# Optimization experiments

Measured on AMD Instinct MI355X. Metric: run time of the kernel, lower is better.

The kernel has to match this reference:

```python
import jax, jax.numpy as jnp
import numpy as np

B, T, D, U = 64, 512, 512, 1024
LN_EPS = 1e-3  # keras LayerNormalization default


def setup_inputs() -> dict:
    key = jax.random.key(0)
    ks = jax.random.split(key, 6)
    s = 0.02
    return {
        "x": jax.random.normal(ks[0], (B, T, D), jnp.float32),
        "W1": jax.random.normal(ks[1], (D, 4 * U), jnp.float32) * s,
        "R1": jax.random.normal(ks[2], (U, 4 * U), jnp.float32) * s,
        "b1": jnp.zeros((4 * U,), jnp.float32),
        "gamma1": jnp.ones((U,), jnp.float32),
        "beta1": jnp.zeros((U,), jnp.float32),
        "W2": jax.random.normal(ks[3], (U, 4 * U), jnp.float32) * s,
        "R2": jax.random.normal(ks[4], (U, 4 * U), jnp.float32) * s,
        "b2": jnp.zeros((4 * U,), jnp.float32),
        "gamma2": jnp.ones((U,), jnp.float32),
        "beta2": jnp.zeros((U,), jnp.float32),
    }


def lstm_linear(x_btd, W, R, b, return_sequences):
    """Keras LSTM with activation=None: i,f,o sigmoid gates, identity candidate/output."""
    units = R.shape[0]
    # Precompute input projection for all timesteps: [B,T,4U]
    zx = jnp.einsum('btd,dk->btk', x_btd, W) + b

    def step(carry, zx_t):
        h, c = carry
        z = zx_t + h @ R  # [B,4U]
        zi, zf, zg, zo = jnp.split(z, 4, axis=-1)
        i = jax.nn.sigmoid(zi)
        f = jax.nn.sigmoid(zf)
        o = jax.nn.sigmoid(zo)
        c = f * c + i * zg          # activation=None -> linear candidate
        h = o * c                   # activation=None -> linear output
        return (h, c), h

    bsz = x_btd.shape[0]
    init = (jnp.zeros((bsz, units), x_btd.dtype), jnp.zeros((bsz, units), x_btd.dtype))
    (h_last, _), hs = jax.lax.scan(step, init, jnp.swapaxes(zx, 0, 1))  # hs: [T,B,U]
    return jnp.swapaxes(hs, 0, 1) if return_sequences else h_last


def layernorm(x, gamma, beta, eps=LN_EPS):
    mu = jnp.mean(x, axis=-1, keepdims=True)
    var = jnp.mean(jnp.square(x - mu), axis=-1, keepdims=True)
    return (x - mu) * jax.lax.rsqrt(var + eps) * gamma + beta


def reference(x, W1, R1, b1, gamma1, beta1, W2, R2, b2, gamma2, beta2):
    # Layer 1: LSTM (return_sequences=True) -> LayerNorm -> tanh
    h = lstm_linear(x, W1, R1, b1, return_sequences=True)   # [B,T,U]
    h = jnp.tanh(layernorm(h, gamma1, beta1))
    # Layer 2: LSTM (return_sequences=False) -> LayerNorm -> tanh
    h = lstm_linear(h, W2, R2, b2, return_sequences=False)  # [B,U]
    h = jnp.tanh(layernorm(h, gamma2, beta2))
    return h
```

## Files before the change

kernel.cpp:

```cpp
#include <hip/hip_runtime.h>
#include <stdint.h>

#define B_ 64
#define T_ 512
#define D_ 512
#define U_ 1024
#define TC 32
#define NCH 16

typedef unsigned short u16;
typedef u16 ushort8  __attribute__((ext_vector_type(8)));
typedef __bf16 bf16x8 __attribute__((ext_vector_type(8)));
typedef float f32x4  __attribute__((ext_vector_type(4)));

static __device__ __forceinline__ u16 f2bf(float f) {
  unsigned u = __builtin_bit_cast(unsigned, f);
  u += 0x7FFFu + ((u >> 16) & 1u);
  return (u16)(u >> 16);
}
static __device__ __forceinline__ float bf2f(u16 h) {
  unsigned u = ((unsigned)h) << 16;
  return __builtin_bit_cast(float, u);
}


__global__ __launch_bounds__(256) void pack_wt(const float* __restrict__ src,
                                               u16* __restrict__ dst, int K) {
  __shared__ float tile[32][33];
  int n0 = blockIdx.x * 32, k0 = blockIdx.y * 32;
  int tx = threadIdx.x, ty = threadIdx.y;
#pragma unroll
  for (int r = 0; r < 4; ++r) {
    int k = k0 + ty + r * 8;
    tile[ty + r * 8][tx] = src[(long)k * 4096 + n0 + tx];
  }
  __syncthreads();
#pragma unroll
  for (int r = 0; r < 4; ++r) {
    int n = n0 + ty + r * 8;
    int np = ((n & 1023) << 2) | (n >> 10);
    dst[(long)np * K + k0 + tx] = f2bf(tile[tx][ty + r * 8]);
  }
}

__global__ __launch_bounds__(256) void pack_bias(const float* __restrict__ b1,
                                                 const float* __restrict__ b2,
                                                 float* __restrict__ bp) {
  int n = blockIdx.x * 256 + threadIdx.x;
  int np = ((n & 1023) << 2) | (n >> 10);
  bp[np] = b1[n];
  bp[4096 + np] = b2[n];
}


template <bool AF32>
__global__ __launch_bounds__(512) void zx_gemm(const void* __restrict__ Av, long sB, long sT,
                                               int K, const u16* __restrict__ Bp,
                                               const float* __restrict__ biasp,
                                               float* __restrict__ zxo) {
  __shared__ __align__(16) u16 Als[128][72];
  __shared__ __align__(16) u16 Bls[128][72];
  const int tid = threadIdx.x;
  const int mt = blockIdx.x, nt = blockIdx.y;
  const int l = tid & 63, w = tid >> 6;
  const int wm = w >> 2, wn = w & 3;
  const int sr = tid >> 2, skq = (tid & 3) * 16;

  const int gr = mt * 128 + sr;
  const int b = gr >> 5, tt = gr & 31;
  const long abase = (long)b * sB + (long)tt * sT;
  const float* Af = (const float*)Av;
  const u16* Ah = (const u16*)Av;

  const int nc = K >> 6;
  float4 raf[4];
  ushort8 rah[2];
  ushort8 rb[2];

  auto gload = [&](int ch) {
    long k0 = (long)ch << 6;
    if constexpr (AF32) {
#pragma unroll
      for (int i = 0; i < 4; ++i)
        raf[i] = *reinterpret_cast<const float4*>(Af + abase + k0 + skq + i * 4);
    } else {
#pragma unroll
      for (int i = 0; i < 2; ++i)
        rah[i] = *reinterpret_cast<const ushort8*>(Ah + abase + k0 + skq + i * 8);
    }
#pragma unroll
    for (int i = 0; i < 2; ++i)
      rb[i] = *reinterpret_cast<const ushort8*>(Bp + (long)(nt * 128 + sr) * K + k0 + skq + i * 8);
  };

  f32x4 acc[4][2];
#pragma unroll
  for (int fm = 0; fm < 4; ++fm)
#pragma unroll
    for (int fn = 0; fn < 2; ++fn) acc[fm][fn] = (f32x4){0.f, 0.f, 0.f, 0.f};

  gload(0);
  for (int ch = 0; ch < nc; ++ch) {
    __syncthreads();
    if constexpr (AF32) {
      const float* pr = (const float*)raf;
      ushort8 lo, hi;
#pragma unroll
      for (int j = 0; j < 8; ++j) { lo[j] = f2bf(pr[j]); hi[j] = f2bf(pr[8 + j]); }
      *reinterpret_cast<ushort8*>(&Als[sr][skq]) = lo;
      *reinterpret_cast<ushort8*>(&Als[sr][skq + 8]) = hi;
    } else {
      *reinterpret_cast<ushort8*>(&Als[sr][skq]) = rah[0];
      *reinterpret_cast<ushort8*>(&Als[sr][skq + 8]) = rah[1];
    }
    *reinterpret_cast<ushort8*>(&Bls[sr][skq]) = rb[0];
    *reinterpret_cast<ushort8*>(&Bls[sr][skq + 8]) = rb[1];
    __syncthreads();
    if (ch + 1 < nc) gload(ch + 1);
#pragma unroll
    for (int ks = 0; ks < 2; ++ks) {
#pragma unroll
      for (int fm = 0; fm < 4; ++fm) {
        bf16x8 a = __builtin_bit_cast(bf16x8,
            *reinterpret_cast<const ushort8*>(&Als[wm * 64 + fm * 16 + (l & 15)][ks * 32 + (l >> 4) * 8]));
#pragma unroll
        for (int fn = 0; fn < 2; ++fn) {
          bf16x8 bb = __builtin_bit_cast(bf16x8,
              *reinterpret_cast<const ushort8*>(&Bls[wn * 32 + fn * 16 + (l & 15)][ks * 32 + (l >> 4) * 8]));
          acc[fm][fn] = __builtin_amdgcn_mfma_f32_16x16x32_bf16(a, bb, acc[fm][fn], 0, 0, 0);
        }
      }
    }
  }

#pragma unroll
  for (int fm = 0; fm < 4; ++fm)
#pragma unroll
    for (int fn = 0; fn < 2; ++fn) {
      int col = nt * 128 + wn * 32 + fn * 16 + (l & 15);
      float bv = biasp[col];
#pragma unroll
      for (int j = 0; j < 4; ++j) {
        int row = mt * 128 + wm * 64 + fm * 16 + (l >> 4) * 4 + j;
        zxo[(long)row * 4096 + col] = acc[fm][fn][j] + bv;
      }
    }
}


__global__ __launch_bounds__(512) void step2(
    const float* __restrict__ zx1, const u16* __restrict__ R1p, float* __restrict__ c1v,
    const u16* __restrict__ h1r, u16* __restrict__ h1w, u16* __restrict__ h1s,
    const float* __restrict__ zx2, const u16* __restrict__ R2p, float* __restrict__ c2v,
    const u16* __restrict__ h2r, u16* __restrict__ h2w,
    int tt, int act1, int act2) {
  const int layer = blockIdx.x >> 7;
  if (layer ? (!act2) : (!act1)) return;

  __shared__ __align__(16) u16 Als[64][136];
  __shared__ __align__(16) u16 Bls[32][136];
  __shared__ float Zls[64][36];

  const float* zx = layer ? zx2 : zx1;
  const u16* Rp   = layer ? R2p : R1p;
  float* cv       = layer ? c2v : c1v;
  const u16* hr   = layer ? h2r : h1r;
  u16* hw         = layer ? h2w : h1w;

  const int cb = blockIdx.x & 127;
  const int n0 = cb * 32;
  const int tid = threadIdx.x;
  const int l = tid & 63, w = tid >> 6;
  const int wm = w >> 1, wn = w & 1;

  const int arow = tid >> 3, ak = (tid & 7) * 16;
  const int brow = tid >> 4, bk = (tid & 15) * 8;

  ushort8 ra0, ra1, rbv;
  auto gload = [&](int ch) {
    const int k0 = ch << 7;
    ra0 = *reinterpret_cast<const ushort8*>(hr + arow * U_ + k0 + ak);
    ra1 = *reinterpret_cast<const ushort8*>(hr + arow * U_ + k0 + ak + 8);
    rbv = *reinterpret_cast<const ushort8*>(Rp + (long)(n0 + brow) * U_ + k0 + bk);
  };

  f32x4 acc = {0.f, 0.f, 0.f, 0.f};
  gload(0);
  for (int ch = 0; ch < 8; ++ch) {
    __syncthreads();
    *reinterpret_cast<ushort8*>(&Als[arow][ak]) = ra0;
    *reinterpret_cast<ushort8*>(&Als[arow][ak + 8]) = ra1;
    *reinterpret_cast<ushort8*>(&Bls[brow][bk]) = rbv;
    __syncthreads();
    if (ch < 7) gload(ch + 1);
#pragma unroll
    for (int ks = 0; ks < 4; ++ks) {
      bf16x8 a = __builtin_bit_cast(bf16x8,
          *reinterpret_cast<const ushort8*>(&Als[wm * 16 + (l & 15)][ks * 32 + (l >> 4) * 8]));
      bf16x8 bb = __builtin_bit_cast(bf16x8,
          *reinterpret_cast<const ushort8*>(&Bls[wn * 16 + (l & 15)][ks * 32 + (l >> 4) * 8]));
      acc = __builtin_amdgcn_mfma_f32_16x16x32_bf16(a, bb, acc, 0, 0, 0);
    }
  }

  {
    int r0 = (l >> 4) * 4, col = wn * 16 + (l & 15);
#pragma unroll
    for (int j = 0; j < 4; ++j) Zls[wm * 16 + r0 + j][col] = acc[j];
  }
  __syncthreads();

  {
    int b = tid >> 3, uu = tid & 7;
    int u = cb * 8 + uu;
    float z0 = Zls[b][uu * 4], z1 = Zls[b][uu * 4 + 1];
    float z2 = Zls[b][uu * 4 + 2], z3 = Zls[b][uu * 4 + 3];
    f32x4 zv = *reinterpret_cast<const f32x4*>(zx + ((long)b * TC + tt) * 4096 + n0 + uu * 4);
    float zi = z0 + zv[0], zf = z1 + zv[1], zg = z2 + zv[2], zo = z3 + zv[3];
    float ig = 1.f / (1.f + expf(-zi));
    float fg = 1.f / (1.f + expf(-zf));
    float og = 1.f / (1.f + expf(-zo));
    long ci = (long)b * U_ + u;
    float cn = fg * cv[ci] + ig * zg;
    cv[ci] = cn;
    u16 hv = f2bf(og * cn);
    hw[ci] = hv;
    if (layer == 0) h1s[(long)b * ((long)T_ * U_) + u] = hv;
  }
}


__global__ __launch_bounds__(256) void ln_chunk(const u16* __restrict__ h1seq, int t0,
                                                const float* __restrict__ gamma,
                                                const float* __restrict__ beta,
                                                u16* __restrict__ dst) {
  __shared__ float sbuf[8];
  int row = blockIdx.x;
  int b = row >> 5, tt = row & 31;
  const u16* src = h1seq + ((long)b * T_ + t0 + tt) * U_;
  u16* drow = dst + (long)row * U_;
  float x[4];
#pragma unroll
  for (int j = 0; j < 4; ++j) x[j] = bf2f(src[threadIdx.x + 256 * j]);
  float s = x[0] + x[1] + x[2] + x[3];
  for (int o = 32; o > 0; o >>= 1) s += __shfl_down(s, o, 64);
  if ((threadIdx.x & 63) == 0) sbuf[threadIdx.x >> 6] = s;
  __syncthreads();
  float mu = (sbuf[0] + sbuf[1] + sbuf[2] + sbuf[3]) * (1.f / 1024.f);
  float d[4], s2 = 0.f;
#pragma unroll
  for (int j = 0; j < 4; ++j) { d[j] = x[j] - mu; s2 += d[j] * d[j]; }
  for (int o = 32; o > 0; o >>= 1) s2 += __shfl_down(s2, o, 64);
  if ((threadIdx.x & 63) == 0) sbuf[4 + (threadIdx.x >> 6)] = s2;
  __syncthreads();
  float inv = rsqrtf((sbuf[4] + sbuf[5] + sbuf[6] + sbuf[7]) * (1.f / 1024.f) + 1e-3f);
#pragma unroll
  for (int j = 0; j < 4; ++j) {
    int u = threadIdx.x + 256 * j;
    drow[u] = f2bf(tanhf(d[j] * inv * gamma[u] + beta[u]));
  }
}

__global__ __launch_bounds__(256) void ln_tanh_final(const u16* __restrict__ h2,
                                                     const float* __restrict__ gamma,
                                                     const float* __restrict__ beta,
                                                     float* __restrict__ out) {
  __shared__ float sbuf[8];
  const u16* row = h2 + (long)blockIdx.x * U_;
  float x[4];
#pragma unroll
  for (int j = 0; j < 4; ++j) x[j] = bf2f(row[threadIdx.x + 256 * j]);
  float s = x[0] + x[1] + x[2] + x[3];
  for (int o = 32; o > 0; o >>= 1) s += __shfl_down(s, o, 64);
  if ((threadIdx.x & 63) == 0) sbuf[threadIdx.x >> 6] = s;
  __syncthreads();
  float mu = (sbuf[0] + sbuf[1] + sbuf[2] + sbuf[3]) * (1.f / 1024.f);
  float d[4], s2 = 0.f;
#pragma unroll
  for (int j = 0; j < 4; ++j) { d[j] = x[j] - mu; s2 += d[j] * d[j]; }
  for (int o = 32; o > 0; o >>= 1) s2 += __shfl_down(s2, o, 64);
  if ((threadIdx.x & 63) == 0) sbuf[4 + (threadIdx.x >> 6)] = s2;
  __syncthreads();
  float inv = rsqrtf((sbuf[4] + sbuf[5] + sbuf[6] + sbuf[7]) * (1.f / 1024.f) + 1e-3f);
#pragma unroll
  for (int j = 0; j < 4; ++j) {
    int u = threadIdx.x + 256 * j;
    out[(long)blockIdx.x * U_ + u] = tanhf(d[j] * inv * gamma[u] + beta[u]);
  }
}


extern "C" void kernel_launch(void* const* d_in, const int* in_sizes, int n_in,
                              void* d_out, int out_size, void* d_ws, size_t ws_size,
                              hipStream_t stream) {
  const float* x      = (const float*)d_in[0];
  const float* W1     = (const float*)d_in[1];
  const float* R1     = (const float*)d_in[2];
  const float* b1     = (const float*)d_in[3];
  const float* gamma1 = (const float*)d_in[4];
  const float* beta1  = (const float*)d_in[5];
  const float* W2     = (const float*)d_in[6];
  const float* R2     = (const float*)d_in[7];
  const float* b2     = (const float*)d_in[8];
  const float* gamma2 = (const float*)d_in[9];
  const float* beta2  = (const float*)d_in[10];
  float* out = (float*)d_out;

  char* base = (char*)d_ws;
  size_t off = 0;
  auto alloc = [&](size_t bytes) -> void* {
    void* p = base + off;
    off += (bytes + 255) & ~(size_t)255;
    return p;
  };
  u16*   Wp1   = (u16*)alloc((size_t)4096 * D_ * 2);
  u16*   Rp1   = (u16*)alloc((size_t)4096 * U_ * 2);
  u16*   Wp2   = (u16*)alloc((size_t)4096 * U_ * 2);
  u16*   Rp2   = (u16*)alloc((size_t)4096 * U_ * 2);
  float* biasp = (float*)alloc((size_t)2 * 4096 * 4);
  float* zxA   = (float*)alloc((size_t)B_ * TC * 4096 * 4);
  float* zxB   = (float*)alloc((size_t)B_ * TC * 4096 * 4);
  u16*   h1seq = (u16*)alloc((size_t)B_ * T_ * U_ * 2);
  u16*   h1ln  = (u16*)alloc((size_t)B_ * TC * U_ * 2);
  float* c1    = (float*)alloc((size_t)B_ * U_ * 4);
  float* c2    = (float*)alloc((size_t)B_ * U_ * 4);
  u16*   h1a   = (u16*)alloc((size_t)B_ * U_ * 2);
  u16*   h1b   = (u16*)alloc((size_t)B_ * U_ * 2);
  u16*   h2a   = (u16*)alloc((size_t)B_ * U_ * 2);
  u16*   h2b   = (u16*)alloc((size_t)B_ * U_ * 2);

  pack_wt<<<dim3(128, 16), dim3(32, 8), 0, stream>>>(W1, Wp1, D_);
  pack_wt<<<dim3(128, 32), dim3(32, 8), 0, stream>>>(R1, Rp1, U_);
  pack_wt<<<dim3(128, 32), dim3(32, 8), 0, stream>>>(W2, Wp2, U_);
  pack_wt<<<dim3(128, 32), dim3(32, 8), 0, stream>>>(R2, Rp2, U_);
  pack_bias<<<16, 256, 0, stream>>>(b1, b2, biasp);
  hipMemsetAsync(c1, 0, (size_t)B_ * U_ * 4, stream);
  hipMemsetAsync(c2, 0, (size_t)B_ * U_ * 4, stream);
  hipMemsetAsync(h1a, 0, (size_t)B_ * U_ * 2, stream);
  hipMemsetAsync(h2a, 0, (size_t)B_ * U_ * 2, stream);

  for (int p = 0; p <= NCH; ++p) {
    int act1 = (p < NCH), act2 = (p >= 1);
    if (act1)
      zx_gemm<true><<<dim3(16, 32), 512, 0, stream>>>(
          (const void*)(x + (long)p * TC * D_), (long)T_ * D_, (long)D_, D_, Wp1, biasp, zxA);
    if (act2) {
      ln_chunk<<<B_ * TC, 256, 0, stream>>>(h1seq, (p - 1) * TC, gamma1, beta1, h1ln);
      zx_gemm<false><<<dim3(16, 32), 512, 0, stream>>>(
          (const void*)h1ln, (long)TC * U_, (long)U_, U_, Wp2, biasp + 4096, zxB);
    }
    for (int tt = 0; tt < TC; ++tt) {
      u16* h1r = (tt & 1) ? h1b : h1a;
      u16* h1w = (tt & 1) ? h1a : h1b;
      u16* h2r = (tt & 1) ? h2b : h2a;
      u16* h2w = (tt & 1) ? h2a : h2b;
      step2<<<256, 512, 0, stream>>>(zxA, Rp1, c1, h1r, h1w,
                                     h1seq + (long)(p * TC + tt) * U_,
                                     zxB, Rp2, c2, h2r, h2w, tt, act1, act2);
    }
  }
  ln_tanh_final<<<B_, 256, 0, stream>>>(h2a, gamma2, beta2, out);
}
```

Measured before the change: 5.370 ms.

## Replace per-timestep launches with persistent cooperative chunk kernel using flag sync

Each 32-step chunk now runs as one cooperative kernel of 256 blocks instead of 32 separate step launches. Blocks synchronize between timesteps through per-step atomic counters that are spin-polled. Each block keeps its cell state in a register and now covers 16 batch rows by 128 gate columns, with double-buffered recurrent-weight tiles. This is meant to remove launch overhead and the round-trip of c through global memory, at the cost of spin-wait latency and a reliance on all blocks being co-resident.

New measurement: 6.276 ms. 16.9% more time.

```diff
diff --git a/kernel.cpp b/kernel.cpp
--- a/kernel.cpp
+++ b/kernel.cpp
@@ -9,6 +9,7 @@
 #define NCH 16
 
 typedef unsigned short u16;
+typedef unsigned long long u64;
 typedef u16 ushort8  __attribute__((ext_vector_type(8)));
 typedef __bf16 bf16x8 __attribute__((ext_vector_type(8)));
 typedef float f32x4  __attribute__((ext_vector_type(4)));
@@ -148,85 +149,129 @@
 }
 
 
-__global__ __launch_bounds__(512) void step2(
+__global__ __launch_bounds__(512) void lstm_chunk(
     const float* __restrict__ zx1, const u16* __restrict__ R1p, float* __restrict__ c1v,
-    const u16* __restrict__ h1r, u16* __restrict__ h1w, u16* __restrict__ h1s,
+    u16* __restrict__ h1_0, u16* __restrict__ h1_1, u16* __restrict__ h1s,
     const float* __restrict__ zx2, const u16* __restrict__ R2p, float* __restrict__ c2v,
-    const u16* __restrict__ h2r, u16* __restrict__ h2w,
-    int tt, int act1, int act2) {
+    u16* __restrict__ h2_0, u16* __restrict__ h2_1,
+    unsigned* __restrict__ flag1, unsigned* __restrict__ flag2,
+    int g01, int g02, int act1, int act2) {
   const int layer = blockIdx.x >> 7;
   if (layer ? (!act2) : (!act1)) return;
 
-  __shared__ __align__(16) u16 Als[64][136];
-  __shared__ __align__(16) u16 Bls[32][136];
-  __shared__ float Zls[64][36];
+  __shared__ __align__(16) u16 Als[16][1032];
+  __shared__ __align__(16) u16 Bls[2][128][136];
+  __shared__ float Zls[16][132];
 
   const float* zx = layer ? zx2 : zx1;
   const u16* Rp   = layer ? R2p : R1p;
   float* cv       = layer ? c2v : c1v;
-  const u16* hr   = layer ? h2r : h1r;
-  u16* hw         = layer ? h2w : h1w;
-
-  const int cb = blockIdx.x & 127;
-  const int n0 = cb * 32;
+  u16* hb0        = layer ? h2_0 : h1_0;
+  u16* hb1        = layer ? h2_1 : h1_1;
+  unsigned* flag  = layer ? flag2 : flag1;
+  const int g0    = layer ? g02 : g01;
+
+  const int lb = blockIdx.x & 127;
+  const int q = lb >> 5;
+  const int cg = lb & 31;
+  const int n0 = cg * 128;
+  const int u0 = cg * 32;
+
   const int tid = threadIdx.x;
   const int l = tid & 63, w = tid >> 6;
-  const int wm = w >> 1, wn = w & 1;
-
-  const int arow = tid >> 3, ak = (tid & 7) * 16;
-  const int brow = tid >> 4, bk = (tid & 15) * 8;
-
-  ushort8 ra0, ra1, rbv;
-  auto gload = [&](int ch) {
-    const int k0 = ch << 7;
-    ra0 = *reinterpret_cast<const ushort8*>(hr + arow * U_ + k0 + ak);
-    ra1 = *reinterpret_cast<const ushort8*>(hr + arow * U_ + k0 + ak + 8);
-    rbv = *reinterpret_cast<const ushort8*>(Rp + (long)(n0 + brow) * U_ + k0 + bk);
+
+  const int tArow = tid >> 5, tAoff = (tid & 31) * 32;
+  const int tBrow = tid >> 2, tBoff = (tid & 3) * 32;
+  const int tgb = tid >> 5, tgun = tid & 31;
+  const int bq = q * 16 + tgb;
+  const int ug = u0 + tgun;
+
+  float creg = cv[(long)bq * U_ + ug];
+
+  ushort8 rbv[4];
+  auto gloadB = [&](int ch) {
+#pragma unroll
+    for (int i = 0; i < 4; ++i)
+      rbv[i] = *reinterpret_cast<const ushort8*>(Rp + (long)(n0 + tBrow) * U_ + ch * 128 + tBoff + i * 8);
   };
 
-  f32x4 acc = {0.f, 0.f, 0.f, 0.f};
-  gload(0);
-  for (int ch = 0; ch < 8; ++ch) {
+  for (int tt = 0; tt < TC; ++tt) {
+    const int g = g0 + tt;
+
+    if (g > 0) {
+      if (tid == 0) {
+        while (__hip_atomic_load(&flag[g - 1], __ATOMIC_RELAXED, __HIP_MEMORY_SCOPE_AGENT) < 128u)
+          __builtin_amdgcn_s_sleep(2);
+      }
+      __syncthreads();
+    }
+
+    const u16* hr = (g & 1) ? hb0 : hb1;
+    u16* hw       = (g & 1) ? hb1 : hb0;
+    {
+      u64* src = (u64*)(hr + (long)(q * 16 + tArow) * U_ + tAoff);
+#pragma unroll
+      for (int i = 0; i < 8; ++i) {
+        u64 v = __hip_atomic_load(src + i, __ATOMIC_RELAXED, __HIP_MEMORY_SCOPE_AGENT);
+        *reinterpret_cast<u64*>(&Als[tArow][tAoff + i * 4]) = v;
+      }
+    }
+
+    f32x4 acc = {0.f, 0.f, 0.f, 0.f};
+    gloadB(0);
+#pragma unroll
+    for (int i = 0; i < 4; ++i)
+      *reinterpret_cast<ushort8*>(&Bls[0][tBrow][tBoff + i * 8]) = rbv[i];
+    for (int ch = 0; ch < 8; ++ch) {
+      if (ch < 7) gloadB(ch + 1);
+      __syncthreads();
+      if (ch < 7) {
+#pragma unroll
+        for (int i = 0; i < 4; ++i)
+          *reinterpret_cast<ushort8*>(&Bls[(ch + 1) & 1][tBrow][tBoff + i * 8]) = rbv[i];
+      }
+#pragma unroll
+      for (int ks = 0; ks < 4; ++ks) {
+        bf16x8 a = __builtin_bit_cast(bf16x8,
+            *reinterpret_cast<const ushort8*>(&Als[l & 15][ch * 128 + ks * 32 + (l >> 4) * 8]));
+        bf16x8 bb = __builtin_bit_cast(bf16x8,
+            *reinterpret_cast<const ushort8*>(&Bls[ch & 1][w * 16 + (l & 15)][ks * 32 + (l >> 4) * 8]));
+        acc = __builtin_amdgcn_mfma_f32_16x16x32_bf16(a, bb, acc, 0, 0, 0);
+      }
+    }
+
+    {
+      int r0 = (l >> 4) * 4, col = w * 16 + (l & 15);
+#pragma unroll
+      for (int j = 0; j < 4; ++j) Zls[r0 + j][col] = acc[j];
+    }
     __syncthreads();
-    *reinterpret_cast<ushort8*>(&Als[arow][ak]) = ra0;
-    *reinterpret_cast<ushort8*>(&Als[arow][ak + 8]) = ra1;
-    *reinterpret_cast<ushort8*>(&Bls[brow][bk]) = rbv;
+
+    {
+      f32x4 zr = *reinterpret_cast<const f32x4*>(&Zls[tgb][tgun * 4]);
+      f32x4 zv = *reinterpret_cast<const f32x4*>(zx + ((long)bq * TC + tt) * 4096 + n0 + tgun * 4);
+      float zi = zr[0] + zv[0], zf = zr[1] + zv[1], zg = zr[2] + zv[2], zo = zr[3] + zv[3];
+      float ig = 1.f / (1.f + expf(-zi));
+      float fg = 1.f / (1.f + expf(-zf));
+      float og = 1.f / (1.f + expf(-zo));
+      creg = fg * creg + ig * zg;
+      u16 hv = f2bf(og * creg);
+      unsigned hvn = __shfl_down((unsigned)hv, 1, 64);
+      if ((tgun & 1) == 0) {
+        unsigned pv = (unsigned)hv | (hvn << 16);
+        __hip_atomic_store((unsigned*)(hw + (long)bq * U_ + ug), pv,
+                           __ATOMIC_RELAXED, __HIP_MEMORY_SCOPE_AGENT);
+      }
+      if (layer == 0) h1s[((long)bq * T_ + g) * U_ + ug] = hv;
+    }
+
+    asm volatile("s_waitcnt vmcnt(0)" ::: "memory");
     __syncthreads();
-    if (ch < 7) gload(ch + 1);
-#pragma unroll
-    for (int ks = 0; ks < 4; ++ks) {
-      bf16x8 a = __builtin_bit_cast(bf16x8,
-          *reinterpret_cast<const ushort8*>(&Als[wm * 16 + (l & 15)][ks * 32 + (l >> 4) * 8]));
-      bf16x8 bb = __builtin_bit_cast(bf16x8,
-          *reinterpret_cast<const ushort8*>(&Bls[wn * 16 + (l & 15)][ks * 32 + (l >> 4) * 8]));
-      acc = __builtin_amdgcn_mfma_f32_16x16x32_bf16(a, bb, acc, 0, 0, 0);
-    }
-  }
-
-  {
-    int r0 = (l >> 4) * 4, col = wn * 16 + (l & 15);
-#pragma unroll
-    for (int j = 0; j < 4; ++j) Zls[wm * 16 + r0 + j][col] = acc[j];
-  }
-  __syncthreads();
-
-  {
-    int b = tid >> 3, uu = tid & 7;
-    int u = cb * 8 + uu;
-    float z0 = Zls[b][uu * 4], z1 = Zls[b][uu * 4 + 1];
-    float z2 = Zls[b][uu * 4 + 2], z3 = Zls[b][uu * 4 + 3];
-    f32x4 zv = *reinterpret_cast<const f32x4*>(zx + ((long)b * TC + tt) * 4096 + n0 + uu * 4);
-    float zi = z0 + zv[0], zf = z1 + zv[1], zg = z2 + zv[2], zo = z3 + zv[3];
-    float ig = 1.f / (1.f + expf(-zi));
-    float fg = 1.f / (1.f + expf(-zf));
-    float og = 1.f / (1.f + expf(-zo));
-    long ci = (long)b * U_ + u;
-    float cn = fg * cv[ci] + ig * zg;
-    cv[ci] = cn;
-    u16 hv = f2bf(og * cn);
-    hw[ci] = hv;
-    if (layer == 0) h1s[(long)b * ((long)T_ * U_) + u] = hv;
-  }
+    if (tid == 0)
+      __hip_atomic_fetch_add(&flag[g], 1u, __ATOMIC_RELAXED, __HIP_MEMORY_SCOPE_AGENT);
+  }
+
+  cv[(long)bq * U_ + ug] = creg;
 }
 
 
@@ -313,21 +358,23 @@
     off += (bytes + 255) & ~(size_t)255;
     return p;
   };
-  u16*   Wp1   = (u16*)alloc((size_t)4096 * D_ * 2);
-  u16*   Rp1   = (u16*)alloc((size_t)4096 * U_ * 2);
-  u16*   Wp2   = (u16*)alloc((size_t)4096 * U_ * 2);
-  u16*   Rp2   = (u16*)alloc((size_t)4096 * U_ * 2);
-  float* biasp = (float*)alloc((size_t)2 * 4096 * 4);
-  float* zxA   = (float*)alloc((size_t)B_ * TC * 4096 * 4);
-  float* zxB   = (float*)alloc((size_t)B_ * TC * 4096 * 4);
-  u16*   h1seq = (u16*)alloc((size_t)B_ * T_ * U_ * 2);
-  u16*   h1ln  = (u16*)alloc((size_t)B_ * TC * U_ * 2);
-  float* c1    = (float*)alloc((size_t)B_ * U_ * 4);
-  float* c2    = (float*)alloc((size_t)B_ * U_ * 4);
-  u16*   h1a   = (u16*)alloc((size_t)B_ * U_ * 2);
-  u16*   h1b   = (u16*)alloc((size_t)B_ * U_ * 2);
-  u16*   h2a   = (u16*)alloc((size_t)B_ * U_ * 2);
-  u16*   h2b   = (u16*)alloc((size_t)B_ * U_ * 2);
+  u16*      Wp1   = (u16*)alloc((size_t)4096 * D_ * 2);
+  u16*      Rp1   = (u16*)alloc((size_t)4096 * U_ * 2);
+  u16*      Wp2   = (u16*)alloc((size_t)4096 * U_ * 2);
+  u16*      Rp2   = (u16*)alloc((size_t)4096 * U_ * 2);
+  float*    biasp = (float*)alloc((size_t)2 * 4096 * 4);
+  float*    zxA   = (float*)alloc((size_t)B_ * TC * 4096 * 4);
+  float*    zxB   = (float*)alloc((size_t)B_ * TC * 4096 * 4);
+  u16*      h1seq = (u16*)alloc((size_t)B_ * T_ * U_ * 2);
+  u16*      h1ln  = (u16*)alloc((size_t)B_ * TC * U_ * 2);
+  float*    c1    = (float*)alloc((size_t)B_ * U_ * 4);
+  float*    c2    = (float*)alloc((size_t)B_ * U_ * 4);
+  u16*      h1a   = (u16*)alloc((size_t)B_ * U_ * 2);
+  u16*      h1b   = (u16*)alloc((size_t)B_ * U_ * 2);
+  u16*      h2a   = (u16*)alloc((size_t)B_ * U_ * 2);
+  u16*      h2b   = (u16*)alloc((size_t)B_ * U_ * 2);
+  unsigned* flag1 = (unsigned*)alloc((size_t)T_ * 4);
+  unsigned* flag2 = (unsigned*)alloc((size_t)T_ * 4);
 
   pack_wt<<<dim3(128, 16), dim3(32, 8), 0, stream>>>(W1, Wp1, D_);
   pack_wt<<<dim3(128, 32), dim3(32, 8), 0, stream>>>(R1, Rp1, U_);
@@ -336,8 +383,10 @@
   pack_bias<<<16, 256, 0, stream>>>(b1, b2, biasp);
   hipMemsetAsync(c1, 0, (size_t)B_ * U_ * 4, stream);
   hipMemsetAsync(c2, 0, (size_t)B_ * U_ * 4, stream);
-  hipMemsetAsync(h1a, 0, (size_t)B_ * U_ * 2, stream);
-  hipMemsetAsync(h2a, 0, (size_t)B_ * U_ * 2, stream);
+  hipMemsetAsync(h1b, 0, (size_t)B_ * U_ * 2, stream);
+  hipMemsetAsync(h2b, 0, (size_t)B_ * U_ * 2, stream);
+  hipMemsetAsync(flag1, 0, (size_t)T_ * 4, stream);
+  hipMemsetAsync(flag2, 0, (size_t)T_ * 4, stream);
 
   for (int p = 0; p <= NCH; ++p) {
     int act1 = (p < NCH), act2 = (p >= 1);
@@ -349,15 +398,16 @@
       zx_gemm<false><<<dim3(16, 32), 512, 0, stream>>>(
           (const void*)h1ln, (long)TC * U_, (long)U_, U_, Wp2, biasp + 4096, zxB);
     }
-    for (int tt = 0; tt < TC; ++tt) {
-      u16* h1r = (tt & 1) ? h1b : h1a;
-      u16* h1w = (tt & 1) ? h1a : h1b;
-      u16* h2r = (tt & 1) ? h2b : h2a;
-      u16* h2w = (tt & 1) ? h2a : h2b;
-      step2<<<256, 512, 0, stream>>>(zxA, Rp1, c1, h1r, h1w,
-                                     h1seq + (long)(p * TC + tt) * U_,
-                                     zxB, Rp2, c2, h2r, h2w, tt, act1, act2);
-    }
-  }
-  ln_tanh_final<<<B_, 256, 0, stream>>>(h2a, gamma2, beta2, out);
-}
+    const float* p_zx1 = zxA; const u16* p_R1 = Rp1; float* p_c1 = c1;
+    u16* p_h10 = h1a; u16* p_h11 = h1b; u16* p_h1s = h1seq;
+    const float* p_zx2 = zxB; const u16* p_R2 = Rp2; float* p_c2 = c2;
+    u16* p_h20 = h2a; u16* p_h21 = h2b;
+    unsigned* p_f1 = flag1; unsigned* p_f2 = flag2;
+    int p_g01 = p * TC, p_g02 = (p - 1) * TC, p_a1 = act1, p_a2 = act2;
+    void* args[17] = {&p_zx1, &p_R1, &p_c1, &p_h10, &p_h11, &p_h1s,
+                      &p_zx2, &p_R2, &p_c2, &p_h20, &p_h21,
+                      &p_f1, &p_f2, &p_g01, &p_g02, &p_a1, &p_a2};
+    hipLaunchCooperativeKernel((void*)lstm_chunk, dim3(256), dim3(512), args, 0, stream);
+  }
+  ln_tanh_final<<<B_, 256, 0, stream>>>(h2b, gamma2, beta2, out);
+}
```
